# Optimization experiments

Measured on AMD Instinct MI355X. Metric: run time of the kernel, lower is better.

Reference implementation:

```python
import jax, jax.numpy as jnp
import numpy as np

BATCH, SEQ, DIM, HEADS, DSTATE, BLOCK = 2, 4096, 1024, 16, 64, 64
LN_EPS = 1e-6

def segsum(x):
    # x: (..., T) -> (..., T, T); segsum[i, j] = sum_{j < k <= i} x[k]; -inf above diagonal
    T = x.shape[-1]
    cs = jnp.cumsum(x, axis=-1)
    seg = cs[..., :, None] - cs[..., None, :]
    mask = jnp.tril(jnp.ones((T, T), dtype=bool))
    return jnp.where(mask, seg, -jnp.inf)

def ssd_minimal_discrete(X, A, C, B, block_len):
    # X: (b,s,h,p) already multiplied by dt; A: (b,s,h) = A*dt; C readout, B input: (b,s,h,n)
    b, s, h, p = X.shape
    n = B.shape[-1]
    c = s // block_len
    l = block_len
    Xc = X.reshape(b, c, l, h, p)
    Bc = B.reshape(b, c, l, h, n)
    Cc = C.reshape(b, c, l, h, n)
    Ac = A.reshape(b, c, l, h).transpose(0, 3, 1, 2)  # (b,h,c,l)
    A_cumsum = jnp.cumsum(Ac, axis=-1)
    # 1. intra-chunk (diagonal block) outputs
    L = jnp.exp(segsum(Ac))  # (b,h,c,l,l)
    Y_diag = jnp.einsum('bclhn,bcshn,bhcls,bcshp->bclhp', Cc, Bc, L, Xc)
    # 2. states at end of each chunk
    decay_states = jnp.exp(A_cumsum[..., -1:] - A_cumsum)
    states = jnp.einsum('bclhn,bhcl,bclhp->bchpn', Bc, decay_states, Xc)
    # 3. inter-chunk recurrence on chunk states
    init = jnp.zeros_like(states[:, :1])
    states = jnp.concatenate([init, states], axis=1)  # (b,c+1,h,p,n)
    decay_chunk = jnp.exp(segsum(jnp.pad(A_cumsum[..., -1], ((0, 0), (0, 0), (1, 0)))))
    new_states = jnp.einsum('bhzc,bchpn->bzhpn', decay_chunk, states)
    states, final_state = new_states[:, :-1], new_states[:, -1]
    # 4. state -> output contribution (off-diagonal blocks)
    state_decay_out = jnp.exp(A_cumsum)
    Y_off = jnp.einsum('bclhn,bchpn,bhcl->bclhp', Cc, states, state_decay_out)
    return (Y_diag + Y_off).reshape(b, s, h, p), final_state

def setup_inputs():
    key = jax.random.key(0)
    ks = jax.random.split(key, 8)
    X = jax.random.normal(ks[0], (BATCH, SEQ, DIM), jnp.float32)
    B = jax.random.normal(ks[1], (BATCH, SEQ, HEADS * DSTATE), jnp.float32)
    C = jax.random.normal(ks[2], (BATCH, SEQ, HEADS * DSTATE), jnp.float32)
    W_dt = jax.random.normal(ks[3], (DIM, HEADS), jnp.float32) * 0.02
    # dt_bias initializer: inverse-softplus of dt ~ LogUniform(1e-3, 1e-1)
    dt = jnp.exp(jax.random.uniform(ks[4], (1, SEQ, HEADS)) * (jnp.log(0.1) - jnp.log(0.001)) + jnp.log(0.001))
    dt = jnp.clip(dt, 1e-4)
    dt_bias = dt + jnp.log(-jnp.expm1(-dt))
    # a_log initializer: log of Uniform(1, 16)
    a_log = jnp.log(jax.random.uniform(ks[5], (HEADS,), minval=1.0, maxval=16.0))
    W_out = jax.random.normal(ks[6], (DIM, DIM), jnp.float32) * 0.02
    ln_scale = jnp.ones((DIM,), jnp.float32)
    ln_bias = jnp.zeros((DIM,), jnp.float32)
    return {"X": X, "B": B, "C": C, "W_dt": W_dt, "dt_bias": dt_bias, "a_log": a_log,
            "W_out": W_out, "ln_scale": ln_scale, "ln_bias": ln_bias, "block_len": BLOCK}

def reference(X, B, C, W_dt, dt_bias, a_log, W_out, ln_scale, ln_bias, block_len):
    b, s, dim = X.shape
    h = a_log.shape[0]
    Xh = X.reshape(b, s, h, -1)
    Bh = B.reshape(b, s, h, -1)
    Ch = C.reshape(b, s, h, -1)
    dt = jax.nn.softplus(jnp.einsum('bsd,dh->bsh', X, W_dt) + dt_bias)  # (b,s,h)
    A = -jnp.exp(a_log)  # (h,)
    y, final_state = ssd_minimal_discrete(Xh * dt[..., None], A * dt, Ch, Bh, block_len)
    y = y.reshape(b, s, dim)
    mu = jnp.mean(y, axis=-1, keepdims=True)
    var = jnp.mean(jnp.square(y - mu), axis=-1, keepdims=True)
    yn = (y - mu) / jnp.sqrt(var + LN_EPS) * ln_scale + ln_bias
    out = jnp.einsum('bsd,de->bse', yn, W_out)
    return out, final_state
```

## Files before the change

kernel.cpp:

```cpp
#include <hip/hip_runtime.h>
#include <hip/hip_bf16.h>
#include <math.h>

#define BATCH   2
#define SEQ     4096
#define DIM     1024
#define HEADS   16
#define DSTATE  64
#define HEADDIM 64
#define BLOCKL  64
#define NCHUNK  64
#define ROWS    (BATCH*SEQ)

typedef __attribute__((ext_vector_type(4))) float f32x4;
typedef __attribute__((ext_vector_type(8))) short bf16x8;

static __device__ __forceinline__ float softplus_f(float x){
    return (x > 20.f) ? x : log1pf(__expf(x));
}
static __device__ __forceinline__ ushort f2b(float f){
    __hip_bfloat16 h = __float2bfloat16(f);
    return *reinterpret_cast<ushort*>(&h);
}

__global__ __launch_bounds__(256) void k_dt(const float* __restrict__ X,
        const float* __restrict__ Wdt, const float* __restrict__ dtb,
        const float* __restrict__ alog,
        float* __restrict__ dt_g, float* __restrict__ dtA_g){
    int r = blockIdx.x;
    int s = r & (SEQ-1);
    int tid = threadIdx.x;
    __shared__ float xrow[DIM];
    __shared__ float red[16][17];
    *(f32x4*)(xrow + tid*4) = *(const f32x4*)(X + (size_t)r*DIM + tid*4);
    __syncthreads();
    int part = tid >> 4, h = tid & 15;
    int d0 = part * 64;
    float acc = 0.f;
    #pragma unroll 8
    for (int i = 0; i < 64; ++i)
        acc += xrow[d0 + i] * Wdt[(size_t)(d0 + i)*HEADS + h];
    red[part][h] = acc;
    __syncthreads();
    if (tid < 16){
        float sum = 0.f;
        #pragma unroll
        for (int p = 0; p < 16; ++p) sum += red[p][tid];
        sum += dtb[(size_t)s*HEADS + tid];
        float dtv = softplus_f(sum);
        dt_g[(size_t)r*HEADS + tid]  = dtv;
        dtA_g[(size_t)r*HEADS + tid] = -__expf(alog[tid]) * dtv;
    }
}

__global__ __launch_bounds__(256) void k_chunk(const float* __restrict__ X,
        const float* __restrict__ Bin, const float* __restrict__ Cin,
        const float* __restrict__ dt_g, const float* __restrict__ dtA_g,
        float* __restrict__ y_g, float* __restrict__ cstate, float* __restrict__ css_g){
    int bid = blockIdx.x;
    int h = bid & 15, c = (bid >> 4) & 63, b = bid >> 10;
    int tid = threadIdx.x;
    int lane = tid & 63, wave = tid >> 6;
    int r0 = b*SEQ + c*BLOCKL;

    __shared__ __align__(16) char region0[2*64*72*2];
    __shared__ __align__(16) ushort XdT [64*72];
    __shared__ __align__(16) ushort WXdT[64*72];
    __shared__ __align__(16) ushort BT  [64*72];
    __shared__ float csh[64], dtsh[64], wsh[64];
    ushort* Cs = (ushort*)region0;
    ushort* Bs = (ushort*)(region0 + 9216);
    float*  Mf = (float*)region0;

    if (tid < 64){
        dtsh[tid] = dt_g[(size_t)(r0 + tid)*HEADS + h];
        float a = dtA_g[(size_t)(r0 + tid)*HEADS + h];
        #pragma unroll
        for (int off = 1; off < 64; off <<= 1){
            float v = __shfl_up(a, off, 64);
            if (tid >= off) a += v;
        }
        csh[tid] = a;
        css_g[(size_t)bid*64 + tid] = a;
    }
    {
        int l  = tid >> 2;
        int c0 = (tid & 3) * 16;
        const float* bp = Bin + (size_t)(r0 + l)*DIM + h*DSTATE + c0;
        const float* cp = Cin + (size_t)(r0 + l)*DIM + h*DSTATE + c0;
        ushort tb[16], tc[16];
        #pragma unroll
        for (int q = 0; q < 4; ++q){
            f32x4 vb = *(const f32x4*)(bp + q*4);
            f32x4 vc = *(const f32x4*)(cp + q*4);
            #pragma unroll
            for (int j = 0; j < 4; ++j){ tb[q*4+j] = f2b(vb[j]); tc[q*4+j] = f2b(vc[j]); }
        }
        *(uint4*)&Bs[l*72 + c0]     = *(uint4*)&tb[0];
        *(uint4*)&Bs[l*72 + c0 + 8] = *(uint4*)&tb[8];
        *(uint4*)&Cs[l*72 + c0]     = *(uint4*)&tc[0];
        *(uint4*)&Cs[l*72 + c0 + 8] = *(uint4*)&tc[8];
    }
    __syncthreads();
    if (tid < 64) wsh[tid] = __expf(csh[63] - csh[tid]);
    __syncthreads();

    {
        int p  = tid >> 2;
        int l0 = (tid & 3) * 16;
        const float* xcol = X   + (size_t)r0*DIM + h*HEADDIM + p;
        const float* bcol = Bin + (size_t)r0*DIM + h*DSTATE  + p;
        ushort tx[16], tw[16], tbt[16];
        #pragma unroll
        for (int i = 0; i < 16; ++i){
            int l = l0 + i;
            float xv = xcol[(size_t)l*DIM] * dtsh[l];
            tx[i]  = f2b(xv);
            tw[i]  = f2b(xv * wsh[l]);
            tbt[i] = f2b(bcol[(size_t)l*DIM]);
        }
        *(uint4*)&XdT [p*72 + l0]     = *(uint4*)&tx[0];
        *(uint4*)&XdT [p*72 + l0 + 8] = *(uint4*)&tx[8];
        *(uint4*)&WXdT[p*72 + l0]     = *(uint4*)&tw[0];
        *(uint4*)&WXdT[p*72 + l0 + 8] = *(uint4*)&tw[8];
        *(uint4*)&BT  [p*72 + l0]     = *(uint4*)&tbt[0];
        *(uint4*)&BT  [p*72 + l0 + 8] = *(uint4*)&tbt[8];
    }
    __syncthreads();

    int arow  = wave*16 + (lane & 15);
    int kof   = (lane >> 4) * 8;
    int rbase = wave*16 + ((lane >> 4) << 2);
    int cl    = lane & 15;

    f32x4 g[4];
    #pragma unroll
    for (int j = 0; j < 4; ++j) g[j] = (f32x4){0.f,0.f,0.f,0.f};
    #pragma unroll
    for (int k = 0; k < 2; ++k){
        bf16x8 a = *(const bf16x8*)&Cs[arow*72 + k*32 + kof];
        #pragma unroll
        for (int j = 0; j < 4; ++j){
            bf16x8 bb = *(const bf16x8*)&Bs[(16*j + (lane&15))*72 + k*32 + kof];
            g[j] = __builtin_amdgcn_mfma_f32_16x16x32_bf16(a, bb, g[j], 0, 0, 0);
        }
    }
    __syncthreads();

    #pragma unroll
    for (int j = 0; j < 4; ++j){
        #pragma unroll
        for (int r = 0; r < 4; ++r){
            int row = rbase + r, col = 16*j + cl;
            float m = 0.f;
            if (col <= row) m = g[j][r] * __expf(csh[row] - csh[col]);
            Mf[row*65 + col] = m;
        }
    }
    __syncthreads();

    f32x4 y[4];
    #pragma unroll
    for (int j = 0; j < 4; ++j) y[j] = (f32x4){0.f,0.f,0.f,0.f};
    #pragma unroll
    for (int k = 0; k < 2; ++k){
        bf16x8 am;
        #pragma unroll
        for (int i = 0; i < 8; ++i)
            am[i] = (short)f2b(Mf[arow*65 + k*32 + kof + i]);
        #pragma unroll
        for (int j = 0; j < 4; ++j){
            bf16x8 bx = *(const bf16x8*)&XdT[(16*j + (lane&15))*72 + k*32 + kof];
            y[j] = __builtin_amdgcn_mfma_f32_16x16x32_bf16(am, bx, y[j], 0, 0, 0);
        }
    }
    #pragma unroll
    for (int j = 0; j < 4; ++j)
        #pragma unroll
        for (int r = 0; r < 4; ++r)
            y_g[(size_t)(r0 + rbase + r)*DIM + h*HEADDIM + 16*j + cl] = y[j][r];

    f32x4 st[4];
    #pragma unroll
    for (int j = 0; j < 4; ++j) st[j] = (f32x4){0.f,0.f,0.f,0.f};
    #pragma unroll
    for (int k = 0; k < 2; ++k){
        bf16x8 aw = *(const bf16x8*)&WXdT[arow*72 + k*32 + kof];
        #pragma unroll
        for (int j = 0; j < 4; ++j){
            bf16x8 bb = *(const bf16x8*)&BT[(16*j + (lane&15))*72 + k*32 + kof];
            st[j] = __builtin_amdgcn_mfma_f32_16x16x32_bf16(aw, bb, st[j], 0, 0, 0);
        }
    }
    #pragma unroll
    for (int j = 0; j < 4; ++j)
        #pragma unroll
        for (int r = 0; r < 4; ++r)
            cstate[(size_t)bid*4096 + (rbase + r)*64 + 16*j + cl] = st[j][r];
}

__global__ __launch_bounds__(256) void k_scan(float* __restrict__ cstate,
        const float* __restrict__ css_g, float* __restrict__ fs_out){
    int bid = blockIdx.x;
    int tile = bid & 15, h = (bid >> 4) & 15, b = bid >> 8;
    int pn = tile*256 + threadIdx.x;
    float P = 0.f;
    for (int c = 0; c < NCHUNK; ++c){
        size_t base = (size_t)((b*NCHUNK + c)*HEADS + h);
        float e   = __expf(css_g[base*64 + 63]);
        float cur = cstate[base*4096 + pn];
        cstate[base*4096 + pn] = P;
        P = e*P + cur;
    }
    fs_out[(size_t)(b*HEADS + h)*4096 + pn] = P;
}

__global__ __launch_bounds__(256) void k_yoff(const float* __restrict__ Cin,
        const float* __restrict__ cstate, const float* __restrict__ css_g,
        float* __restrict__ y_g){
    int bid = blockIdx.x;
    int h = bid & 15, c = (bid >> 4) & 63, b = bid >> 10;
    int tid = threadIdx.x;
    int lane = tid & 63, wave = tid >> 6;
    int r0 = b*SEQ + c*BLOCKL;
    __shared__ __align__(16) ushort Cs[64*72];
    __shared__ __align__(16) ushort Ss[64*72];
    __shared__ float cse[64];
    {
        int l  = tid >> 2;
        int c0 = (tid & 3) * 16;
        const float* cp = Cin    + (size_t)(r0 + l)*DIM + h*DSTATE + c0;
        const float* sp = cstate + (size_t)bid*4096 + l*64 + c0;
        ushort tc[16], ts[16];
        #pragma unroll
        for (int q = 0; q < 4; ++q){
            f32x4 vc = *(const f32x4*)(cp + q*4);
            f32x4 vs = *(const f32x4*)(sp + q*4);
            #pragma unroll
            for (int j = 0; j < 4; ++j){ tc[q*4+j] = f2b(vc[j]); ts[q*4+j] = f2b(vs[j]); }
        }
        *(uint4*)&Cs[l*72 + c0]     = *(uint4*)&tc[0];
        *(uint4*)&Cs[l*72 + c0 + 8] = *(uint4*)&tc[8];
        *(uint4*)&Ss[l*72 + c0]     = *(uint4*)&ts[0];
        *(uint4*)&Ss[l*72 + c0 + 8] = *(uint4*)&ts[8];
    }
    if (tid < 64) cse[tid] = __expf(css_g[(size_t)bid*64 + tid]);
    __syncthreads();

    int arow = wave*16 + (lane & 15);
    int kof  = (lane >> 4) * 8;
    f32x4 acc[4];
    #pragma unroll
    for (int j = 0; j < 4; ++j) acc[j] = (f32x4){0.f,0.f,0.f,0.f};
    #pragma unroll
    for (int k = 0; k < 2; ++k){
        bf16x8 a = *(const bf16x8*)&Cs[arow*72 + k*32 + kof];
        #pragma unroll
        for (int j = 0; j < 4; ++j){
            bf16x8 bb = *(const bf16x8*)&Ss[(16*j + (lane&15))*72 + k*32 + kof];
            acc[j] = __builtin_amdgcn_mfma_f32_16x16x32_bf16(a, bb, acc[j], 0, 0, 0);
        }
    }
    int rbase = wave*16 + ((lane >> 4) << 2);
    int cl = lane & 15;
    #pragma unroll
    for (int j = 0; j < 4; ++j)
        #pragma unroll
        for (int r = 0; r < 4; ++r){
            float e = cse[rbase + r];
            float* yp = y_g + (size_t)(r0 + rbase + r)*DIM + h*HEADDIM + 16*j + cl;
            *yp += e * acc[j][r];
        }
}

__global__ __launch_bounds__(256) void k_ln(const float* __restrict__ y_g,
        const float* __restrict__ scale, const float* __restrict__ bias,
        __hip_bfloat16* __restrict__ yn){
    int r = blockIdx.x, tid = threadIdx.x;
    const float* yp = y_g + (size_t)r*DIM;
    f32x4 v = *(const f32x4*)(yp + tid*4);
    float s1 = v.x + v.y + v.z + v.w;
    float s2 = v.x*v.x + v.y*v.y + v.z*v.z + v.w*v.w;
    #pragma unroll
    for (int m = 32; m > 0; m >>= 1){
        s1 += __shfl_xor(s1, m, 64);
        s2 += __shfl_xor(s2, m, 64);
    }
    __shared__ float w1[4], w2[4];
    int wv = tid >> 6;
    if ((tid & 63) == 0){ w1[wv] = s1; w2[wv] = s2; }
    __syncthreads();
    float S1 = w1[0]+w1[1]+w1[2]+w1[3];
    float S2 = w2[0]+w2[1]+w2[2]+w2[3];
    float mu  = S1 * (1.f/DIM);
    float var = S2 * (1.f/DIM) - mu*mu;
    float rstd = rsqrtf(var + 1e-6f);
    int d = tid*4;
    f32x4 sc = *(const f32x4*)(scale + d);
    f32x4 bi = *(const f32x4*)(bias + d);
    union { __hip_bfloat16 h[4]; short4 s4; } u;
    u.h[0] = __float2bfloat16((v.x - mu)*rstd*sc.x + bi.x);
    u.h[1] = __float2bfloat16((v.y - mu)*rstd*sc.y + bi.y);
    u.h[2] = __float2bfloat16((v.z - mu)*rstd*sc.z + bi.z);
    u.h[3] = __float2bfloat16((v.w - mu)*rstd*sc.w + bi.w);
    *(short4*)((short*)yn + (size_t)r*DIM + d) = u.s4;
}

__global__ __launch_bounds__(256) void k_wt(const float* __restrict__ W,
        __hip_bfloat16* __restrict__ Wt){
    __shared__ float t[64][65];
    int kt = blockIdx.x >> 4, nt = blockIdx.x & 15;
    int tid = threadIdx.x;
    int lr = tid >> 4, lc4 = (tid & 15) * 4;
    #pragma unroll
    for (int q = 0; q < 4; ++q){
        int k = lr + q*16;
        *(f32x4*)&t[k][lc4] = *(const f32x4*)(W + (size_t)(kt*64 + k)*DIM + nt*64 + lc4);
    }
    __syncthreads();
    #pragma unroll
    for (int q = 0; q < 4; ++q){
        int n = lr + q*16;
        union { __hip_bfloat16 h[4]; short4 s4; } u;
        #pragma unroll
        for (int j = 0; j < 4; ++j) u.h[j] = __float2bfloat16(t[lc4+j][n]);
        *(short4*)((short*)Wt + (size_t)(nt*64 + n)*DIM + kt*64 + lc4) = u.s4;
    }
}

__global__ __launch_bounds__(256) void k_gemm(const __hip_bfloat16* __restrict__ A,
        const __hip_bfloat16* __restrict__ Bt, float* __restrict__ Out){
    __shared__ ushort As[128*32];
    __shared__ ushort Bsh[128*32];
    int bid = blockIdx.x;
    int bn = bid & 7, bm = bid >> 3;
    int tid = threadIdx.x;
    int lane = tid & 63, wave = tid >> 6;
    int wr = wave >> 1, wc = wave & 1;
    f32x4 acc[4][4];
    #pragma unroll
    for (int i = 0; i < 4; ++i)
        #pragma unroll
        for (int j = 0; j < 4; ++j)
            acc[i][j] = (f32x4){0.f, 0.f, 0.f, 0.f};
    const ushort* Ag = (const ushort*)A  + (size_t)bm*128*1024;
    const ushort* Bg = (const ushort*)Bt + (size_t)bn*128*1024;
    int row0 = tid >> 2;
    int col0 = (tid & 3) * 8;
    for (int k0 = 0; k0 < 1024; k0 += 32){
        #pragma unroll
        for (int pass = 0; pass < 2; ++pass){
            int row = row0 + pass*64;
            *(uint4*)&As[row*32 + col0]  = *(const uint4*)(Ag + (size_t)row*1024 + k0 + col0);
            *(uint4*)&Bsh[row*32 + col0] = *(const uint4*)(Bg + (size_t)row*1024 + k0 + col0);
        }
        __syncthreads();
        bf16x8 af[4], bfr[4];
        #pragma unroll
        for (int i = 0; i < 4; ++i){
            int arow = wr*64 + i*16 + (lane & 15);
            af[i] = *(const bf16x8*)&As[arow*32 + ((lane >> 4) << 3)];
        }
        #pragma unroll
        for (int j = 0; j < 4; ++j){
            int brow = wc*64 + j*16 + (lane & 15);
            bfr[j] = *(const bf16x8*)&Bsh[brow*32 + ((lane >> 4) << 3)];
        }
        #pragma unroll
        for (int i = 0; i < 4; ++i)
            #pragma unroll
            for (int j = 0; j < 4; ++j)
                acc[i][j] = __builtin_amdgcn_mfma_f32_16x16x32_bf16(af[i], bfr[j], acc[i][j], 0, 0, 0);
        __syncthreads();
    }
    #pragma unroll
    for (int i = 0; i < 4; ++i){
        int m0 = bm*128 + wr*64 + i*16 + ((lane >> 4) << 2);
        #pragma unroll
        for (int j = 0; j < 4; ++j){
            int n = bn*128 + wc*64 + j*16 + (lane & 15);
            #pragma unroll
            for (int reg = 0; reg < 4; ++reg)
                Out[(size_t)(m0 + reg)*1024 + n] = acc[i][j][reg];
        }
    }
}

extern "C" void kernel_launch(void* const* d_in, const int* in_sizes, int n_in,
                              void* d_out, int out_size, void* d_ws, size_t ws_size,
                              hipStream_t stream){
    const float* X    = (const float*)d_in[0];
    const float* Bin  = (const float*)d_in[1];
    const float* Cin  = (const float*)d_in[2];
    const float* Wdt  = (const float*)d_in[3];
    const float* dtb  = (const float*)d_in[4];
    const float* alog = (const float*)d_in[5];
    const float* Wout = (const float*)d_in[6];
    const float* lns  = (const float*)d_in[7];
    const float* lnb  = (const float*)d_in[8];

    float* out = (float*)d_out;
    float* y_g = out;
    float* fs_out = out + (size_t)ROWS*DIM;

    float* dt_g   = (float*)d_ws;
    float* dtA_g  = dt_g  + 131072;
    float* css_g  = dtA_g + 131072;
    float* cstate = css_g + 131072;
    __hip_bfloat16* yn = (__hip_bfloat16*)(cstate + 8388608);
    __hip_bfloat16* Wt = yn + (size_t)ROWS*DIM;

    k_dt   <<<ROWS,          256, 0, stream>>>(X, Wdt, dtb, alog, dt_g, dtA_g);
    k_chunk<<<BATCH*NCHUNK*HEADS, 256, 0, stream>>>(X, Bin, Cin, dt_g, dtA_g, y_g, cstate, css_g);
    k_scan <<<BATCH*HEADS*16, 256, 0, stream>>>(cstate, css_g, fs_out);
    k_yoff <<<BATCH*NCHUNK*HEADS, 256, 0, stream>>>(Cin, cstate, css_g, y_g);
    k_ln   <<<ROWS,          256, 0, stream>>>(y_g, lns, lnb, yn);
    k_wt   <<<256,           256, 0, stream>>>(Wout, Wt);
    k_gemm <<<512,           256, 0, stream>>>(yn, Wt, out);
}
```

Before: 137.4 us.

## Fuse off-diagonal output with layernorm, store chunk states in fp16, use direct-to-LDS loads

Merges the y_off and layernorm kernels into one that computes the state-to-output term with fp16 dot2 instructions and then normalizes the rows in registers. This removes a read-modify-write of y and one launch. Chunk states are now stored as fp16, halving their memory traffic in chunk, scan and output, and the scan handles two elements per thread. k_chunk now reads X/B/C rows in a coalesced pattern and transposes them in LDS instead of doing strided column loads. The GEMM stages its tiles through global_load_lds, which adds precision risk from fp16 states and a possible sync hazard with the async LDS writes.

```diff
diff --git a/kernel.cpp b/kernel.cpp
--- a/kernel.cpp
+++ b/kernel.cpp
@@ -1,5 +1,6 @@
 #include <hip/hip_runtime.h>
 #include <hip/hip_bf16.h>
+#include <hip/hip_fp16.h>
 #include <math.h>
 
 #define BATCH   2
@@ -14,6 +15,7 @@
 
 typedef __attribute__((ext_vector_type(4))) float f32x4;
 typedef __attribute__((ext_vector_type(8))) short bf16x8;
+typedef __attribute__((ext_vector_type(2))) _Float16 f16x2;
 
 static __device__ __forceinline__ float softplus_f(float x){
     return (x > 20.f) ? x : log1pf(__expf(x));
@@ -21,6 +23,20 @@
 static __device__ __forceinline__ ushort f2b(float f){
     __hip_bfloat16 h = __float2bfloat16(f);
     return *reinterpret_cast<ushort*>(&h);
+}
+static __device__ __forceinline__ float fdot2u(uint a, uint b, float c){
+#if __has_builtin(__builtin_amdgcn_fdot2)
+    union { uint u; f16x2 h; } ua, ub; ua.u = a; ub.u = b;
+    return __builtin_amdgcn_fdot2(ua.h, ub.h, c, false);
+#else
+    union { uint u; __half2 h; } ua, ub; ua.u = a; ub.u = b;
+    float2 fa = __half22float2(ua.h), fb = __half22float2(ub.h);
+    return c + fa.x*fb.x + fa.y*fb.y;
+#endif
+}
+static __device__ __forceinline__ void gload16(const void* g, void* l){
+    __builtin_amdgcn_global_load_lds((const __attribute__((address_space(1))) unsigned int*)g,
+                                     (__attribute__((address_space(3))) unsigned int*)l, 16, 0, 0);
 }
 
 __global__ __launch_bounds__(256) void k_dt(const float* __restrict__ X,
@@ -56,14 +72,14 @@
 __global__ __launch_bounds__(256) void k_chunk(const float* __restrict__ X,
         const float* __restrict__ Bin, const float* __restrict__ Cin,
         const float* __restrict__ dt_g, const float* __restrict__ dtA_g,
-        float* __restrict__ y_g, float* __restrict__ cstate, float* __restrict__ css_g){
+        float* __restrict__ y_g, ushort* __restrict__ cstate, float* __restrict__ css_g){
     int bid = blockIdx.x;
     int h = bid & 15, c = (bid >> 4) & 63, b = bid >> 10;
     int tid = threadIdx.x;
     int lane = tid & 63, wave = tid >> 6;
     int r0 = b*SEQ + c*BLOCKL;
 
-    __shared__ __align__(16) char region0[2*64*72*2];
+    __shared__ __align__(16) char region0[18432];
     __shared__ __align__(16) ushort XdT [64*72];
     __shared__ __align__(16) ushort WXdT[64*72];
     __shared__ __align__(16) ushort BT  [64*72];
@@ -72,6 +88,21 @@
     ushort* Bs = (ushort*)(region0 + 9216);
     float*  Mf = (float*)region0;
 
+    int l  = tid >> 2;
+    int c0 = (tid & 3) * 16;
+
+    f32x4 xr[4], br[4], cr[4];
+    {
+        const float* xp = X   + (size_t)(r0 + l)*DIM + h*HEADDIM + c0;
+        const float* bp = Bin + (size_t)(r0 + l)*DIM + h*DSTATE  + c0;
+        const float* cp = Cin + (size_t)(r0 + l)*DIM + h*DSTATE  + c0;
+        #pragma unroll
+        for (int q = 0; q < 4; ++q){
+            xr[q] = *(const f32x4*)(xp + q*4);
+            br[q] = *(const f32x4*)(bp + q*4);
+            cr[q] = *(const f32x4*)(cp + q*4);
+        }
+    }
     if (tid < 64){
         dtsh[tid] = dt_g[(size_t)(r0 + tid)*HEADS + h];
         float a = dtA_g[(size_t)(r0 + tid)*HEADS + h];
@@ -82,67 +113,54 @@
         }
         csh[tid] = a;
         css_g[(size_t)bid*64 + tid] = a;
-    }
+        float cs63 = __shfl(a, 63, 64);
+        wsh[tid] = __expf(cs63 - a);
+    }
+    ushort tc[16], tb[16];
+    #pragma unroll
+    for (int q = 0; q < 4; ++q)
+        #pragma unroll
+        for (int j = 0; j < 4; ++j){
+            tc[q*4+j] = f2b(cr[q][j]);
+            tb[q*4+j] = f2b(br[q][j]);
+        }
+    *(uint4*)&Cs[l*72 + c0]     = *(uint4*)&tc[0];
+    *(uint4*)&Cs[l*72 + c0 + 8] = *(uint4*)&tc[8];
+    *(uint4*)&Bs[l*72 + c0]     = *(uint4*)&tb[0];
+    *(uint4*)&Bs[l*72 + c0 + 8] = *(uint4*)&tb[8];
+    __syncthreads();
+
     {
-        int l  = tid >> 2;
-        int c0 = (tid & 3) * 16;
-        const float* bp = Bin + (size_t)(r0 + l)*DIM + h*DSTATE + c0;
-        const float* cp = Cin + (size_t)(r0 + l)*DIM + h*DSTATE + c0;
-        ushort tb[16], tc[16];
-        #pragma unroll
-        for (int q = 0; q < 4; ++q){
-            f32x4 vb = *(const f32x4*)(bp + q*4);
-            f32x4 vc = *(const f32x4*)(cp + q*4);
+        float dl = dtsh[l], wl = wsh[l];
+        #pragma unroll
+        for (int q = 0; q < 4; ++q)
             #pragma unroll
-            for (int j = 0; j < 4; ++j){ tb[q*4+j] = f2b(vb[j]); tc[q*4+j] = f2b(vc[j]); }
-        }
-        *(uint4*)&Bs[l*72 + c0]     = *(uint4*)&tb[0];
-        *(uint4*)&Bs[l*72 + c0 + 8] = *(uint4*)&tb[8];
-        *(uint4*)&Cs[l*72 + c0]     = *(uint4*)&tc[0];
-        *(uint4*)&Cs[l*72 + c0 + 8] = *(uint4*)&tc[8];
-    }
-    __syncthreads();
-    if (tid < 64) wsh[tid] = __expf(csh[63] - csh[tid]);
-    __syncthreads();
-
-    {
-        int p  = tid >> 2;
-        int l0 = (tid & 3) * 16;
-        const float* xcol = X   + (size_t)r0*DIM + h*HEADDIM + p;
-        const float* bcol = Bin + (size_t)r0*DIM + h*DSTATE  + p;
-        ushort tx[16], tw[16], tbt[16];
-        #pragma unroll
-        for (int i = 0; i < 16; ++i){
-            int l = l0 + i;
-            float xv = xcol[(size_t)l*DIM] * dtsh[l];
-            tx[i]  = f2b(xv);
-            tw[i]  = f2b(xv * wsh[l]);
-            tbt[i] = f2b(bcol[(size_t)l*DIM]);
-        }
-        *(uint4*)&XdT [p*72 + l0]     = *(uint4*)&tx[0];
-        *(uint4*)&XdT [p*72 + l0 + 8] = *(uint4*)&tx[8];
-        *(uint4*)&WXdT[p*72 + l0]     = *(uint4*)&tw[0];
-        *(uint4*)&WXdT[p*72 + l0 + 8] = *(uint4*)&tw[8];
-        *(uint4*)&BT  [p*72 + l0]     = *(uint4*)&tbt[0];
-        *(uint4*)&BT  [p*72 + l0 + 8] = *(uint4*)&tbt[8];
-    }
-    __syncthreads();
-
-    int arow  = wave*16 + (lane & 15);
-    int kof   = (lane >> 4) * 8;
-    int rbase = wave*16 + ((lane >> 4) << 2);
-    int cl    = lane & 15;
-
-    f32x4 g[4];
-    #pragma unroll
-    for (int j = 0; j < 4; ++j) g[j] = (f32x4){0.f,0.f,0.f,0.f};
+            for (int j = 0; j < 4; ++j){
+                int p = c0 + q*4 + j;
+                float xv = xr[q][j] * dl;
+                XdT [p*72 + l] = f2b(xv);
+                WXdT[p*72 + l] = f2b(xv * wl);
+                BT  [p*72 + l] = tb[q*4+j];
+            }
+    }
+    __syncthreads();
+
+    int cl15  = lane & 15;
+    int g     = lane >> 4;
+    int arow  = wave*16 + cl15;
+    int kof   = g * 8;
+    int rbase = wave*16 + g*4;
+
+    f32x4 gacc[4];
+    #pragma unroll
+    for (int j = 0; j < 4; ++j) gacc[j] = (f32x4){0.f,0.f,0.f,0.f};
     #pragma unroll
     for (int k = 0; k < 2; ++k){
         bf16x8 a = *(const bf16x8*)&Cs[arow*72 + k*32 + kof];
         #pragma unroll
         for (int j = 0; j < 4; ++j){
-            bf16x8 bb = *(const bf16x8*)&Bs[(16*j + (lane&15))*72 + k*32 + kof];
-            g[j] = __builtin_amdgcn_mfma_f32_16x16x32_bf16(a, bb, g[j], 0, 0, 0);
+            bf16x8 bb = *(const bf16x8*)&Bs[(16*j + cl15)*72 + k*32 + kof];
+            gacc[j] = __builtin_amdgcn_mfma_f32_16x16x32_bf16(a, bb, gacc[j], 0, 0, 0);
         }
     }
     __syncthreads();
@@ -151,9 +169,9 @@
     for (int j = 0; j < 4; ++j){
         #pragma unroll
         for (int r = 0; r < 4; ++r){
-            int row = rbase + r, col = 16*j + cl;
+            int row = rbase + r, col = 16*j + cl15;
             float m = 0.f;
-            if (col <= row) m = g[j][r] * __expf(csh[row] - csh[col]);
+            if (col <= row) m = gacc[j][r] * __expf(csh[row] - csh[col]);
             Mf[row*65 + col] = m;
         }
     }
@@ -170,7 +188,7 @@
             am[i] = (short)f2b(Mf[arow*65 + k*32 + kof + i]);
         #pragma unroll
         for (int j = 0; j < 4; ++j){
-            bf16x8 bx = *(const bf16x8*)&XdT[(16*j + (lane&15))*72 + k*32 + kof];
+            bf16x8 bx = *(const bf16x8*)&XdT[(16*j + cl15)*72 + k*32 + kof];
             y[j] = __builtin_amdgcn_mfma_f32_16x16x32_bf16(am, bx, y[j], 0, 0, 0);
         }
     }
@@ -178,7 +196,7 @@
     for (int j = 0; j < 4; ++j)
         #pragma unroll
         for (int r = 0; r < 4; ++r)
-            y_g[(size_t)(r0 + rbase + r)*DIM + h*HEADDIM + 16*j + cl] = y[j][r];
+            y_g[(size_t)(r0 + rbase + r)*DIM + h*HEADDIM + 16*j + cl15] = y[j][r];
 
     f32x4 st[4];
     #pragma unroll
@@ -188,122 +206,127 @@
         bf16x8 aw = *(const bf16x8*)&WXdT[arow*72 + k*32 + kof];
         #pragma unroll
         for (int j = 0; j < 4; ++j){
-            bf16x8 bb = *(const bf16x8*)&BT[(16*j + (lane&15))*72 + k*32 + kof];
+            bf16x8 bb = *(const bf16x8*)&BT[(16*j + cl15)*72 + k*32 + kof];
             st[j] = __builtin_amdgcn_mfma_f32_16x16x32_bf16(aw, bb, st[j], 0, 0, 0);
         }
     }
     #pragma unroll
     for (int j = 0; j < 4; ++j)
         #pragma unroll
-        for (int r = 0; r < 4; ++r)
-            cstate[(size_t)bid*4096 + (rbase + r)*64 + 16*j + cl] = st[j][r];
-}
-
-__global__ __launch_bounds__(256) void k_scan(float* __restrict__ cstate,
+        for (int r = 0; r < 4; ++r){
+            __half hv = __float2half(st[j][r]);
+            cstate[(size_t)bid*4096 + (size_t)(rbase + r)*64 + 16*j + cl15] = *(ushort*)&hv;
+        }
+}
+
+__global__ __launch_bounds__(256) void k_scan(ushort* __restrict__ cstate,
         const float* __restrict__ css_g, float* __restrict__ fs_out){
     int bid = blockIdx.x;
-    int tile = bid & 15, h = (bid >> 4) & 15, b = bid >> 8;
-    int pn = tile*256 + threadIdx.x;
-    float P = 0.f;
+    int tile = bid & 7, hh = (bid >> 3) & 15, b = bid >> 7;
+    int pn = tile*512 + threadIdx.x*2;
+    float P0 = 0.f, P1 = 0.f;
     for (int c = 0; c < NCHUNK; ++c){
-        size_t base = (size_t)((b*NCHUNK + c)*HEADS + h);
-        float e   = __expf(css_g[base*64 + 63]);
-        float cur = cstate[base*4096 + pn];
-        cstate[base*4096 + pn] = P;
-        P = e*P + cur;
-    }
-    fs_out[(size_t)(b*HEADS + h)*4096 + pn] = P;
-}
-
-__global__ __launch_bounds__(256) void k_yoff(const float* __restrict__ Cin,
-        const float* __restrict__ cstate, const float* __restrict__ css_g,
-        float* __restrict__ y_g){
-    int bid = blockIdx.x;
-    int h = bid & 15, c = (bid >> 4) & 63, b = bid >> 10;
+        size_t base = (size_t)((b*NCHUNK + c)*HEADS + hh);
+        float e = __expf(css_g[base*64 + 63]);
+        __half2 cur = *(const __half2*)&cstate[base*4096 + pn];
+        *( __half2*)&cstate[base*4096 + pn] = __floats2half2_rn(P0, P1);
+        float2 cf = __half22float2(cur);
+        P0 = e*P0 + cf.x;
+        P1 = e*P1 + cf.y;
+    }
+    *(float2*)&fs_out[(size_t)(b*HEADS + hh)*4096 + pn] = make_float2(P0, P1);
+}
+
+__global__ __launch_bounds__(256) void k_yln(const float* __restrict__ Cin,
+        const ushort* __restrict__ cstate, const float* __restrict__ css_g,
+        const float* __restrict__ y_g, const float* __restrict__ scale,
+        const float* __restrict__ bias, __hip_bfloat16* __restrict__ yn){
+    int blk = blockIdx.x;
+    int lg = blk & 7, ch = (blk >> 3) & 63, b = blk >> 9;
     int tid = threadIdx.x;
     int lane = tid & 63, wave = tid >> 6;
-    int r0 = b*SEQ + c*BLOCKL;
-    __shared__ __align__(16) ushort Cs[64*72];
-    __shared__ __align__(16) ushort Ss[64*72];
-    __shared__ float cse[64];
-    {
-        int l  = tid >> 2;
-        int c0 = (tid & 3) * 16;
-        const float* cp = Cin    + (size_t)(r0 + l)*DIM + h*DSTATE + c0;
-        const float* sp = cstate + (size_t)bid*4096 + l*64 + c0;
-        ushort tc[16], ts[16];
-        #pragma unroll
-        for (int q = 0; q < 4; ++q){
-            f32x4 vc = *(const f32x4*)(cp + q*4);
-            f32x4 vs = *(const f32x4*)(sp + q*4);
+    int h = tid >> 4;
+    int r0 = b*SEQ + ch*BLOCKL + lg*8;
+
+    __shared__ uint Crow[8][16*33 + 1];
+    __shared__ float eh2[8][16];
+    __shared__ float r1s[8][5], r2s[8][5];
+
+    #pragma unroll
+    for (int lr = 0; lr < 8; ++lr){
+        f32x4 cv = *(const f32x4*)(Cin + (size_t)(r0 + lr)*DIM + tid*4);
+        __half2 p0 = __floats2half2_rn(cv.x, cv.y);
+        __half2 p1 = __floats2half2_rn(cv.z, cv.w);
+        Crow[lr][h*33 + (tid & 15)*2]     = *(uint*)&p0;
+        Crow[lr][h*33 + (tid & 15)*2 + 1] = *(uint*)&p1;
+    }
+    if (tid < 128){
+        int lr = tid >> 4, hq = tid & 15;
+        eh2[lr][hq] = __expf(css_g[(size_t)(((b*64 + ch)*16 + hq))*64 + lg*8 + lr]);
+    }
+    float yy[8][4];
+    #pragma unroll
+    for (int lr = 0; lr < 8; ++lr){
+        f32x4 yv = *(const f32x4*)(y_g + (size_t)(r0 + lr)*DIM + tid*4);
+        yy[lr][0] = yv.x; yy[lr][1] = yv.y; yy[lr][2] = yv.z; yy[lr][3] = yv.w;
+    }
+    __syncthreads();
+
+    const ushort* Sb = cstate + (size_t)(((b*64 + ch)*16 + h))*4096;
+    int p00 = (tid & 15)*4;
+    #pragma unroll
+    for (int j = 0; j < 4; ++j){
+        const uint4* Sp = (const uint4*)(Sb + (size_t)(p00 + j)*64);
+        uint4 sv[8];
+        #pragma unroll
+        for (int q = 0; q < 8; ++q) sv[q] = Sp[q];
+        #pragma unroll
+        for (int lr = 0; lr < 8; ++lr){
+            float acc = 0.f;
             #pragma unroll
-            for (int j = 0; j < 4; ++j){ tc[q*4+j] = f2b(vc[j]); ts[q*4+j] = f2b(vs[j]); }
-        }
-        *(uint4*)&Cs[l*72 + c0]     = *(uint4*)&tc[0];
-        *(uint4*)&Cs[l*72 + c0 + 8] = *(uint4*)&tc[8];
-        *(uint4*)&Ss[l*72 + c0]     = *(uint4*)&ts[0];
-        *(uint4*)&Ss[l*72 + c0 + 8] = *(uint4*)&ts[8];
-    }
-    if (tid < 64) cse[tid] = __expf(css_g[(size_t)bid*64 + tid]);
-    __syncthreads();
-
-    int arow = wave*16 + (lane & 15);
-    int kof  = (lane >> 4) * 8;
-    f32x4 acc[4];
-    #pragma unroll
-    for (int j = 0; j < 4; ++j) acc[j] = (f32x4){0.f,0.f,0.f,0.f};
-    #pragma unroll
-    for (int k = 0; k < 2; ++k){
-        bf16x8 a = *(const bf16x8*)&Cs[arow*72 + k*32 + kof];
-        #pragma unroll
-        for (int j = 0; j < 4; ++j){
-            bf16x8 bb = *(const bf16x8*)&Ss[(16*j + (lane&15))*72 + k*32 + kof];
-            acc[j] = __builtin_amdgcn_mfma_f32_16x16x32_bf16(a, bb, acc[j], 0, 0, 0);
-        }
-    }
-    int rbase = wave*16 + ((lane >> 4) << 2);
-    int cl = lane & 15;
-    #pragma unroll
-    for (int j = 0; j < 4; ++j)
-        #pragma unroll
-        for (int r = 0; r < 4; ++r){
-            float e = cse[rbase + r];
-            float* yp = y_g + (size_t)(r0 + rbase + r)*DIM + h*HEADDIM + 16*j + cl;
-            *yp += e * acc[j][r];
-        }
-}
-
-__global__ __launch_bounds__(256) void k_ln(const float* __restrict__ y_g,
-        const float* __restrict__ scale, const float* __restrict__ bias,
-        __hip_bfloat16* __restrict__ yn){
-    int r = blockIdx.x, tid = threadIdx.x;
-    const float* yp = y_g + (size_t)r*DIM;
-    f32x4 v = *(const f32x4*)(yp + tid*4);
-    float s1 = v.x + v.y + v.z + v.w;
-    float s2 = v.x*v.x + v.y*v.y + v.z*v.z + v.w*v.w;
-    #pragma unroll
-    for (int m = 32; m > 0; m >>= 1){
-        s1 += __shfl_xor(s1, m, 64);
-        s2 += __shfl_xor(s2, m, 64);
-    }
-    __shared__ float w1[4], w2[4];
-    int wv = tid >> 6;
-    if ((tid & 63) == 0){ w1[wv] = s1; w2[wv] = s2; }
-    __syncthreads();
-    float S1 = w1[0]+w1[1]+w1[2]+w1[3];
-    float S2 = w2[0]+w2[1]+w2[2]+w2[3];
-    float mu  = S1 * (1.f/DIM);
-    float var = S2 * (1.f/DIM) - mu*mu;
-    float rstd = rsqrtf(var + 1e-6f);
-    int d = tid*4;
-    f32x4 sc = *(const f32x4*)(scale + d);
-    f32x4 bi = *(const f32x4*)(bias + d);
-    union { __hip_bfloat16 h[4]; short4 s4; } u;
-    u.h[0] = __float2bfloat16((v.x - mu)*rstd*sc.x + bi.x);
-    u.h[1] = __float2bfloat16((v.y - mu)*rstd*sc.y + bi.y);
-    u.h[2] = __float2bfloat16((v.z - mu)*rstd*sc.z + bi.z);
-    u.h[3] = __float2bfloat16((v.w - mu)*rstd*sc.w + bi.w);
-    *(short4*)((short*)yn + (size_t)r*DIM + d) = u.s4;
+            for (int q = 0; q < 8; ++q){
+                acc = fdot2u(sv[q].x, Crow[lr][h*33 + q*4 + 0], acc);
+                acc = fdot2u(sv[q].y, Crow[lr][h*33 + q*4 + 1], acc);
+                acc = fdot2u(sv[q].z, Crow[lr][h*33 + q*4 + 2], acc);
+                acc = fdot2u(sv[q].w, Crow[lr][h*33 + q*4 + 3], acc);
+            }
+            yy[lr][j] += eh2[lr][h] * acc;
+        }
+    }
+
+    float mu[8], rs[8];
+    #pragma unroll
+    for (int lr = 0; lr < 8; ++lr){
+        float s1 = yy[lr][0] + yy[lr][1] + yy[lr][2] + yy[lr][3];
+        float s2 = yy[lr][0]*yy[lr][0] + yy[lr][1]*yy[lr][1]
+                 + yy[lr][2]*yy[lr][2] + yy[lr][3]*yy[lr][3];
+        #pragma unroll
+        for (int m = 32; m > 0; m >>= 1){
+            s1 += __shfl_xor(s1, m, 64);
+            s2 += __shfl_xor(s2, m, 64);
+        }
+        if (lane == 0){ r1s[lr][wave] = s1; r2s[lr][wave] = s2; }
+    }
+    __syncthreads();
+    #pragma unroll
+    for (int lr = 0; lr < 8; ++lr){
+        float S1 = r1s[lr][0] + r1s[lr][1] + r1s[lr][2] + r1s[lr][3];
+        float S2 = r2s[lr][0] + r2s[lr][1] + r2s[lr][2] + r2s[lr][3];
+        float m_ = S1 * (1.f/DIM);
+        float v_ = S2 * (1.f/DIM) - m_*m_;
+        mu[lr] = m_;
+        rs[lr] = rsqrtf(v_ + 1e-6f);
+    }
+    f32x4 sc = *(const f32x4*)(scale + tid*4);
+    f32x4 bi = *(const f32x4*)(bias + tid*4);
+    #pragma unroll
+    for (int lr = 0; lr < 8; ++lr){
+        union { __hip_bfloat16 hh[4]; short4 s4; } u;
+        #pragma unroll
+        for (int j = 0; j < 4; ++j)
+            u.hh[j] = __float2bfloat16((yy[lr][j] - mu[lr])*rs[lr]*sc[j] + bi[j]);
+        *(short4*)((short*)yn + (size_t)(r0 + lr)*DIM + tid*4) = u.s4;
+    }
 }
 
 __global__ __launch_bounds__(256) void k_wt(const float* __restrict__ W,
@@ -330,8 +353,8 @@
 
 __global__ __launch_bounds__(256) void k_gemm(const __hip_bfloat16* __restrict__ A,
         const __hip_bfloat16* __restrict__ Bt, float* __restrict__ Out){
-    __shared__ ushort As[128*32];
-    __shared__ ushort Bsh[128*32];
+    __shared__ __align__(16) ushort As[128*32];
+    __shared__ __align__(16) ushort Bsh[128*32];
     int bid = blockIdx.x;
     int bn = bid & 7, bm = bid >> 3;
     int tid = threadIdx.x;
@@ -348,12 +371,12 @@
     int row0 = tid >> 2;
     int col0 = (tid & 3) * 8;
     for (int k0 = 0; k0 < 1024; k0 += 32){
-        #pragma unroll
-        for (int pass = 0; pass < 2; ++pass){
-            int row = row0 + pass*64;
-            *(uint4*)&As[row*32 + col0]  = *(const uint4*)(Ag + (size_t)row*1024 + k0 + col0);
-            *(uint4*)&Bsh[row*32 + col0] = *(const uint4*)(Bg + (size_t)row*1024 + k0 + col0);
-        }
+        const ushort* sA = Ag + (size_t)row0*1024 + k0 + col0;
+        const ushort* sB = Bg + (size_t)row0*1024 + k0 + col0;
+        gload16(sA,           &As[row0*32 + col0]);
+        gload16(sA + 64*1024, &As[(row0+64)*32 + col0]);
+        gload16(sB,           &Bsh[row0*32 + col0]);
+        gload16(sB + 64*1024, &Bsh[(row0+64)*32 + col0]);
         __syncthreads();
         bf16x8 af[4], bfr[4];
         #pragma unroll
@@ -406,15 +429,14 @@
     float* dt_g   = (float*)d_ws;
     float* dtA_g  = dt_g  + 131072;
     float* css_g  = dtA_g + 131072;
-    float* cstate = css_g + 131072;
+    ushort* cstate = (ushort*)(css_g + 131072);
     __hip_bfloat16* yn = (__hip_bfloat16*)(cstate + 8388608);
     __hip_bfloat16* Wt = yn + (size_t)ROWS*DIM;
 
-    k_dt   <<<ROWS,          256, 0, stream>>>(X, Wdt, dtb, alog, dt_g, dtA_g);
+    k_dt   <<<ROWS,               256, 0, stream>>>(X, Wdt, dtb, alog, dt_g, dtA_g);
     k_chunk<<<BATCH*NCHUNK*HEADS, 256, 0, stream>>>(X, Bin, Cin, dt_g, dtA_g, y_g, cstate, css_g);
-    k_scan <<<BATCH*HEADS*16, 256, 0, stream>>>(cstate, css_g, fs_out);
-    k_yoff <<<BATCH*NCHUNK*HEADS, 256, 0, stream>>>(Cin, cstate, css_g, y_g);
-    k_ln   <<<ROWS,          256, 0, stream>>>(y_g, lns, lnb, yn);
-    k_wt   <<<256,           256, 0, stream>>>(Wout, Wt);
-    k_gemm <<<512,           256, 0, stream>>>(yn, Wt, out);
-}
+    k_scan <<<BATCH*HEADS*8,      256, 0, stream>>>(cstate, css_g, fs_out);
+    k_yln  <<<BATCH*NCHUNK*8,     256, 0, stream>>>(Cin, cstate, css_g, y_g, lns, lnb, yn);
+    k_wt   <<<256,                256, 0, stream>>>(Wout, Wt);
+    k_gemm <<<512,                256, 0, stream>>>(yn, Wt, out);
+}
```

Measured after the change: 167.9 us. 22.2% more time.
